# Performance work log

Measured on AMD Instinct MI355X. Metric: run time of the kernel, lower is better.

Reference implementation:

```python
import jax, jax.numpy as jnp
import numpy as np

B, H, S, D = 2, 12, 2048, 64

def setup_inputs() -> dict:
    key = jax.random.key(0)
    kq, kk, kv = jax.random.split(key, 3)
    Q = jax.random.normal(kq, (B, H, S, D), dtype=jnp.float32)
    K = jax.random.normal(kk, (B, H, S, D), dtype=jnp.float32)
    V = jax.random.normal(kv, (B, H, S, D), dtype=jnp.float32)
    return {"Q": Q, "K": K, "V": V}

def reference(Q, K, V):
    # NOTE: original code scales by sqrt(Q.shape[-2]) (the sequence length),
    # not the head dim — reproduced faithfully.
    scale = 1.0 / np.sqrt(Q.shape[-2]).astype(np.float32)
    scores = jnp.einsum('bhqd,bhkd->bhqk', Q, K) * scale  # [B,H,S,S]
    attn = jax.nn.softmax(scores, axis=-1)
    context = jnp.einsum('bhqk,bhkd->bhqd', attn, V)      # [B,H,S,D]
    # torch .squeeze(-1) only removes the last dim if it is size 1; D=64 so no-op
    return context
```

## Files before the change

kernel.cpp:

```cpp
#include <hip/hip_runtime.h>
#include <math.h>
#include <stdint.h>

#define BATCH 2
#define NH 12
#define SEQ 2048
#define HD 64
#define TQ 64
#define TK 64
#define NHEADS (BATCH*NH)
#define NIT (SEQ / TK)

typedef short bf16x8 __attribute__((ext_vector_type(8)));
typedef float f32x4 __attribute__((ext_vector_type(4)));
typedef unsigned short us8_t __attribute__((ext_vector_type(8)));

#if __has_builtin(__builtin_amdgcn_exp2f)
#define EXP2F(x) __builtin_amdgcn_exp2f(x)
#else
#define EXP2F(x) exp2f(x)
#endif

static __device__ __forceinline__ unsigned short f2bf(float f) {
    unsigned int u = __float_as_uint(f);
    u += 0x7fffu + ((u >> 16) & 1u);
    return (unsigned short)(u >> 16);
}

static __device__ __forceinline__ void async_cp16(const void* g, void* l) {
    __builtin_amdgcn_global_load_lds(
        (const __attribute__((address_space(1))) void*)g,
        (__attribute__((address_space(3))) void*)(uintptr_t)l,
        16, 0, 0);
}

__global__ __launch_bounds__(256)
void prep_kv(const float* __restrict__ K, const float* __restrict__ V,
             unsigned short* __restrict__ Kb, unsigned short* __restrict__ Vtb) {
    const int bh = blockIdx.x >> 5;
    const int s0 = (blockIdx.x & 31) * 64;
    const int tid = threadIdx.x;

    const float* Ksrc = K + ((size_t)bh * SEQ + s0) * HD;
    unsigned short* Kdst = Kb + ((size_t)bh * SEQ + s0) * HD;
    #pragma unroll
    for (int i = 0; i < 2; ++i) {
        int e0 = (tid + 256 * i) * 8;
        float4 a = *(const float4*)&Ksrc[e0];
        float4 b = *(const float4*)&Ksrc[e0 + 4];
        us8_t r = { f2bf(a.x), f2bf(a.y), f2bf(a.z), f2bf(a.w),
                    f2bf(b.x), f2bf(b.y), f2bf(b.z), f2bf(b.w) };
        *(us8_t*)&Kdst[e0] = r;
    }

    const float* Vsrc = V + ((size_t)bh * SEQ + s0) * HD;
    unsigned short* Vdst = Vtb + (size_t)bh * HD * SEQ;
    const int n  = tid & 63;
    const int cg = tid >> 6;
    #pragma unroll
    for (int i = 0; i < 4; ++i) {
        int c4 = (cg + 4 * i) * 4;
        float4 v = *(const float4*)&Vsrc[(size_t)n * HD + c4];
        Vdst[(size_t)(c4 + 0) * SEQ + s0 + n] = f2bf(v.x);
        Vdst[(size_t)(c4 + 1) * SEQ + s0 + n] = f2bf(v.y);
        Vdst[(size_t)(c4 + 2) * SEQ + s0 + n] = f2bf(v.z);
        Vdst[(size_t)(c4 + 3) * SEQ + s0 + n] = f2bf(v.w);
    }
}

__global__ __launch_bounds__(256)
void fa_main(const float* __restrict__ Q,
             const unsigned short* __restrict__ Kb,
             const unsigned short* __restrict__ Vtb,
             float* __restrict__ O, float qs) {
    const int x  = blockIdx.x & 7;
    const int t  = blockIdx.x >> 3;
    const int bh = x + 8 * (t % 3);
    const int qt = t / 3;
    const int q0 = qt * TQ;

    __shared__ unsigned short Qs[TQ * HD];
    __shared__ unsigned short Kdb[2][TK * HD];
    __shared__ unsigned short Vdb[2][HD * TK];
    __shared__ unsigned short Ps[4][16][72];

    const int tid   = threadIdx.x;
    const int w     = tid >> 6;
    const int lane  = tid & 63;
    const int col   = lane & 15;
    const int quad  = lane >> 4;
    const int rloc  = lane >> 3;
    const int cphys = lane & 7;
    const int swz   = col & 7;
    const int R     = w * 16;

    const float*          Qh = Q   + ((size_t)bh * SEQ + q0) * HD;
    const unsigned short* Kh = Kb  + (size_t)bh * SEQ * HD;
    const unsigned short* Vh = Vtb + (size_t)bh * HD * SEQ;

    #pragma unroll
    for (int i = 0; i < 2; ++i) {
        int c   = tid * 2 + i;
        int row = c >> 3;
        int ch  = c & 7;
        const float* src = &Qh[(size_t)row * HD + ch * 8];
        float4 a = *(const float4*)&src[0];
        float4 b = *(const float4*)&src[4];
        us8_t r = { f2bf(a.x*qs), f2bf(a.y*qs), f2bf(a.z*qs), f2bf(a.w*qs),
                    f2bf(b.x*qs), f2bf(b.y*qs), f2bf(b.z*qs), f2bf(b.w*qs) };
        *(us8_t*)&Qs[row * HD + ((ch ^ (row & 7)) * 8)] = r;
    }

    {
        async_cp16(Kh + (size_t)(0 + R     + rloc) * HD  + (cphys ^ rloc) * 8, &Kdb[0][ R      * HD]);
        async_cp16(Kh + (size_t)(0 + R + 8 + rloc) * HD  + (cphys ^ rloc) * 8, &Kdb[0][(R + 8) * HD]);
        async_cp16(Vh + (size_t)(R     + rloc) * SEQ + 0 + (cphys ^ rloc) * 8, &Vdb[0][ R      * TK]);
        async_cp16(Vh + (size_t)(R + 8 + rloc) * SEQ + 0 + (cphys ^ rloc) * 8, &Vdb[0][(R + 8) * TK]);
    }
    __syncthreads();

    bf16x8 aq0 = *(const bf16x8*)&Qs[(R + col) * HD + ((quad       ^ swz) * 8)];
    bf16x8 aq1 = *(const bf16x8*)&Qs[(R + col) * HD + (((quad + 4) ^ swz) * 8)];

    f32x4 o[4];
    #pragma unroll
    for (int nt = 0; nt < 4; ++nt) o[nt] = (f32x4){0.f, 0.f, 0.f, 0.f};
    float lsum[4] = {0.f, 0.f, 0.f, 0.f};

    for (int it = 0; it < NIT; ++it) {
        const int cur = it & 1;
        if (it + 1 < NIT) {
            const int nb  = cur ^ 1;
            const int kv0 = (it + 1) * TK;
            async_cp16(Kh + (size_t)(kv0 + R     + rloc) * HD  + (cphys ^ rloc) * 8, &Kdb[nb][ R      * HD]);
            async_cp16(Kh + (size_t)(kv0 + R + 8 + rloc) * HD  + (cphys ^ rloc) * 8, &Kdb[nb][(R + 8) * HD]);
            async_cp16(Vh + (size_t)(R     + rloc) * SEQ + kv0 + (cphys ^ rloc) * 8, &Vdb[nb][ R      * TK]);
            async_cp16(Vh + (size_t)(R + 8 + rloc) * SEQ + kv0 + (cphys ^ rloc) * 8, &Vdb[nb][(R + 8) * TK]);
        }
        const unsigned short* Ks = Kdb[cur];
        const unsigned short* Vs = Vdb[cur];

        f32x4 sc[4];
        #pragma unroll
        for (int nt = 0; nt < 4; ++nt) {
            const int br = nt * 16 + col;
            bf16x8 bk0 = *(const bf16x8*)&Ks[br * HD + ((quad       ^ swz) * 8)];
            bf16x8 bk1 = *(const bf16x8*)&Ks[br * HD + (((quad + 4) ^ swz) * 8)];
            f32x4 z = {0.f, 0.f, 0.f, 0.f};
            z = __builtin_amdgcn_mfma_f32_16x16x32_bf16(aq0, bk0, z, 0, 0, 0);
            z = __builtin_amdgcn_mfma_f32_16x16x32_bf16(aq1, bk1, z, 0, 0, 0);
            sc[nt] = z;
        }

        #pragma unroll
        for (int nt = 0; nt < 4; ++nt) {
            #pragma unroll
            for (int r = 0; r < 4; ++r) {
                float p = EXP2F(sc[nt][r]);
                lsum[r] += p;
                Ps[w][quad * 4 + r][nt * 16 + col] = f2bf(p);
            }
        }

        bf16x8 ap0 = *(const bf16x8*)&Ps[w][col][quad * 8];
        bf16x8 ap1 = *(const bf16x8*)&Ps[w][col][32 + quad * 8];
        #pragma unroll
        for (int nt = 0; nt < 4; ++nt) {
            const int br = nt * 16 + col;
            bf16x8 bv0 = *(const bf16x8*)&Vs[br * TK + ((quad       ^ swz) * 8)];
            bf16x8 bv1 = *(const bf16x8*)&Vs[br * TK + (((quad + 4) ^ swz) * 8)];
            o[nt] = __builtin_amdgcn_mfma_f32_16x16x32_bf16(ap0, bv0, o[nt], 0, 0, 0);
            o[nt] = __builtin_amdgcn_mfma_f32_16x16x32_bf16(ap1, bv1, o[nt], 0, 0, 0);
        }

        __syncthreads();
    }

    #pragma unroll
    for (int off = 1; off < 16; off <<= 1)
        #pragma unroll
        for (int r = 0; r < 4; ++r) lsum[r] += __shfl_xor(lsum[r], off, 64);

    float inv[4];
    #pragma unroll
    for (int r = 0; r < 4; ++r) inv[r] = 1.0f / lsum[r];

    float* Oh = O + ((size_t)bh * SEQ + q0) * HD;
    #pragma unroll
    for (int r = 0; r < 4; ++r) {
        size_t row = (size_t)(R + quad * 4 + r) * HD;
        Oh[row +  0 + col] = o[0][r] * inv[r];
        Oh[row + 16 + col] = o[1][r] * inv[r];
        Oh[row + 32 + col] = o[2][r] * inv[r];
        Oh[row + 48 + col] = o[3][r] * inv[r];
    }
}

#define PAD 8
#define LSTR (HD + PAD)

__global__ __launch_bounds__(256)
void fa_fwd_fb(const float* __restrict__ Q, const float* __restrict__ K,
               const float* __restrict__ V, float* __restrict__ O) {
    const int x  = blockIdx.x & 7;
    const int t  = blockIdx.x >> 3;
    const int bh = x + 8 * (t % 3);
    const int qt = t / 3;
    const int q0 = qt * TQ;
    const long base = (long)bh * SEQ * HD;

    __shared__ unsigned short Qs[TQ][LSTR];
    __shared__ unsigned short Ks2[TK][LSTR];
    __shared__ unsigned short Vt[HD][TK + PAD];
    __shared__ unsigned short Ps2[4][16][LSTR];

    const int tid  = threadIdx.x;
    const int wave = tid >> 6;
    const int lane = tid & 63;
    const int col  = lane & 15;
    const int quad = lane >> 4;
    const int m0   = wave * 16;

    #pragma unroll
    for (int i = 0; i < 4; ++i) {
        int idx = tid + 256 * i;
        int row = idx >> 4;
        int c4  = (idx & 15) * 4;
        float4 v = *(const float4*)&Q[base + (long)(q0 + row) * HD + c4];
        ushort4 b = { f2bf(v.x), f2bf(v.y), f2bf(v.z), f2bf(v.w) };
        *(ushort4*)&Qs[row][c4] = b;
    }
    __syncthreads();

    bf16x8 aq0 = *(const bf16x8*)&Qs[m0 + col][quad * 8];
    bf16x8 aq1 = *(const bf16x8*)&Qs[m0 + col][32 + quad * 8];

    f32x4 o0 = {0.f,0.f,0.f,0.f}, o1 = o0, o2 = o0, o3 = o0;
    float l[4] = {0.f, 0.f, 0.f, 0.f};
    const float scale = 0.022097086912079608f;

    for (int kv0 = 0; kv0 < SEQ; kv0 += TK) {
        __syncthreads();
        #pragma unroll
        for (int i = 0; i < 4; ++i) {
            int idx = tid + 256 * i;
            int row = idx >> 4;
            int c4  = (idx & 15) * 4;
            float4 kv = *(const float4*)&K[base + (long)(kv0 + row) * HD + c4];
            ushort4 kb = { f2bf(kv.x), f2bf(kv.y), f2bf(kv.z), f2bf(kv.w) };
            *(ushort4*)&Ks2[row][c4] = kb;
            float4 vv = *(const float4*)&V[base + (long)(kv0 + row) * HD + c4];
            Vt[c4 + 0][row] = f2bf(vv.x);
            Vt[c4 + 1][row] = f2bf(vv.y);
            Vt[c4 + 2][row] = f2bf(vv.z);
            Vt[c4 + 3][row] = f2bf(vv.w);
        }
        __syncthreads();

        f32x4 sc[4];
        #pragma unroll
        for (int n = 0; n < 4; ++n) {
            bf16x8 b0 = *(const bf16x8*)&Ks2[n * 16 + col][quad * 8];
            bf16x8 b1 = *(const bf16x8*)&Ks2[n * 16 + col][32 + quad * 8];
            f32x4 acc = {0.f,0.f,0.f,0.f};
            acc = __builtin_amdgcn_mfma_f32_16x16x32_bf16(aq0, b0, acc, 0, 0, 0);
            acc = __builtin_amdgcn_mfma_f32_16x16x32_bf16(aq1, b1, acc, 0, 0, 0);
            sc[n] = acc;
        }

        float tsum[4] = {0.f, 0.f, 0.f, 0.f};
        #pragma unroll
        for (int n = 0; n < 4; ++n) {
            #pragma unroll
            for (int r = 0; r < 4; ++r) {
                float p = __expf(sc[n][r] * scale);
                tsum[r] += p;
                Ps2[wave][quad * 4 + r][n * 16 + col] = f2bf(p);
            }
        }
        #pragma unroll
        for (int off = 1; off < 16; off <<= 1) {
            #pragma unroll
            for (int r = 0; r < 4; ++r) tsum[r] += __shfl_xor(tsum[r], off, 64);
        }
        #pragma unroll
        for (int r = 0; r < 4; ++r) l[r] += tsum[r];

        bf16x8 ap0 = *(const bf16x8*)&Ps2[wave][col][quad * 8];
        bf16x8 ap1 = *(const bf16x8*)&Ps2[wave][col][32 + quad * 8];
        #pragma unroll
        for (int n = 0; n < 4; ++n) {
            bf16x8 b0 = *(const bf16x8*)&Vt[n * 16 + col][quad * 8];
            bf16x8 b1 = *(const bf16x8*)&Vt[n * 16 + col][32 + quad * 8];
            f32x4* op = (n == 0) ? &o0 : (n == 1) ? &o1 : (n == 2) ? &o2 : &o3;
            *op = __builtin_amdgcn_mfma_f32_16x16x32_bf16(ap0, b0, *op, 0, 0, 0);
            *op = __builtin_amdgcn_mfma_f32_16x16x32_bf16(ap1, b1, *op, 0, 0, 0);
        }
    }

    float inv[4];
    #pragma unroll
    for (int r = 0; r < 4; ++r) inv[r] = 1.0f / l[r];
    #pragma unroll
    for (int r = 0; r < 4; ++r) {
        long row = base + (long)(q0 + m0 + quad * 4 + r) * HD;
        O[row +  0 + col] = o0[r] * inv[r];
        O[row + 16 + col] = o1[r] * inv[r];
        O[row + 32 + col] = o2[r] * inv[r];
        O[row + 48 + col] = o3[r] * inv[r];
    }
}

extern "C" void kernel_launch(void* const* d_in, const int* in_sizes, int n_in,
                              void* d_out, int out_size, void* d_ws, size_t ws_size,
                              hipStream_t stream) {
    const float* Q = (const float*)d_in[0];
    const float* K = (const float*)d_in[1];
    const float* V = (const float*)d_in[2];
    float* O = (float*)d_out;

    const size_t tensorElems = (size_t)NHEADS * SEQ * HD;
    const size_t need = 2 * tensorElems * sizeof(unsigned short);

    if (ws_size >= need) {
        unsigned short* Kb  = (unsigned short*)d_ws;
        unsigned short* Vtb = Kb + tensorElems;
        const float qs = (float)(1.4426950408889634 / sqrt(2048.0));
        prep_kv<<<dim3(NHEADS * (SEQ / 64)), dim3(256), 0, stream>>>(K, V, Kb, Vtb);
        fa_main<<<dim3(NHEADS * (SEQ / TQ)), dim3(256), 0, stream>>>(Q, Kb, Vtb, O, qs);
    } else {
        fa_fwd_fb<<<dim3(NHEADS * (SEQ / TQ)), dim3(256), 0, stream>>>(Q, K, V, O);
    }
}
```

Baseline: 130.5 us.

## Use two-wave blocks with 32 query rows per wave and single-buffered KV

Main attention kernel now runs 128 threads per block, each wave handling 32 query rows (two M tiles), so every K/V fragment loaded from LDS feeds twice as many MFMAs. The QK product is computed transposed (K as A operand), which lets P be written with packed bf16x4 stores. Q is converted to bf16 and pre-scaled in the prep kernel, and its LDS buffer is reused for P. K/V double buffering is dropped in favour of a single buffer reloaded between two barriers, which exposes load latency unless other resident blocks hide it.

```diff
diff --git a/kernel.cpp b/kernel.cpp
--- a/kernel.cpp
+++ b/kernel.cpp
@@ -1,4 +1,5 @@
 #include <hip/hip_runtime.h>
+#include <hip/hip_bf16.h>
 #include <math.h>
 #include <stdint.h>
 
@@ -27,6 +28,11 @@
     return (unsigned short)(u >> 16);
 }
 
+static __device__ __forceinline__ unsigned int pack2bf(float a, float b) {
+    __hip_bfloat162 v = __float22bfloat162_rn(float2{a, b});
+    return *(unsigned int*)&v;
+}
+
 static __device__ __forceinline__ void async_cp16(const void* g, void* l) {
     __builtin_amdgcn_global_load_lds(
         (const __attribute__((address_space(1))) void*)g,
@@ -35,25 +41,31 @@
 }
 
 __global__ __launch_bounds__(256)
-void prep_kv(const float* __restrict__ K, const float* __restrict__ V,
-             unsigned short* __restrict__ Kb, unsigned short* __restrict__ Vtb) {
+void prep_qkv(const float* __restrict__ Q, const float* __restrict__ K,
+              const float* __restrict__ V,
+              unsigned short* __restrict__ Qb, unsigned short* __restrict__ Kb,
+              unsigned short* __restrict__ Vtb, float qs) {
     const int bh = blockIdx.x >> 5;
     const int s0 = (blockIdx.x & 31) * 64;
     const int tid = threadIdx.x;
-
-    const float* Ksrc = K + ((size_t)bh * SEQ + s0) * HD;
-    unsigned short* Kdst = Kb + ((size_t)bh * SEQ + s0) * HD;
+    const size_t off = ((size_t)bh * SEQ + s0) * HD;
+
     #pragma unroll
     for (int i = 0; i < 2; ++i) {
-        int e0 = (tid + 256 * i) * 8;
-        float4 a = *(const float4*)&Ksrc[e0];
-        float4 b = *(const float4*)&Ksrc[e0 + 4];
-        us8_t r = { f2bf(a.x), f2bf(a.y), f2bf(a.z), f2bf(a.w),
-                    f2bf(b.x), f2bf(b.y), f2bf(b.z), f2bf(b.w) };
-        *(us8_t*)&Kdst[e0] = r;
-    }
-
-    const float* Vsrc = V + ((size_t)bh * SEQ + s0) * HD;
+        size_t e0 = off + (size_t)(tid + 256 * i) * 8;
+        float4 a = *(const float4*)&Q[e0];
+        float4 b = *(const float4*)&Q[e0 + 4];
+        us8_t rq = { f2bf(a.x*qs), f2bf(a.y*qs), f2bf(a.z*qs), f2bf(a.w*qs),
+                     f2bf(b.x*qs), f2bf(b.y*qs), f2bf(b.z*qs), f2bf(b.w*qs) };
+        *(us8_t*)&Qb[e0] = rq;
+        float4 c = *(const float4*)&K[e0];
+        float4 d = *(const float4*)&K[e0 + 4];
+        us8_t rk = { f2bf(c.x), f2bf(c.y), f2bf(c.z), f2bf(c.w),
+                     f2bf(d.x), f2bf(d.y), f2bf(d.z), f2bf(d.w) };
+        *(us8_t*)&Kb[e0] = rk;
+    }
+
+    const float* Vsrc = V + off;
     unsigned short* Vdst = Vtb + (size_t)bh * HD * SEQ;
     const int n  = tid & 63;
     const int cg = tid >> 6;
@@ -68,131 +80,146 @@
     }
 }
 
-__global__ __launch_bounds__(256)
-void fa_main(const float* __restrict__ Q,
+__global__ __launch_bounds__(128)
+void fa_main(const unsigned short* __restrict__ Qb,
              const unsigned short* __restrict__ Kb,
              const unsigned short* __restrict__ Vtb,
-             float* __restrict__ O, float qs) {
+             float* __restrict__ O) {
     const int x  = blockIdx.x & 7;
     const int t  = blockIdx.x >> 3;
     const int bh = x + 8 * (t % 3);
     const int qt = t / 3;
     const int q0 = qt * TQ;
 
-    __shared__ unsigned short Qs[TQ * HD];
-    __shared__ unsigned short Kdb[2][TK * HD];
-    __shared__ unsigned short Vdb[2][HD * TK];
-    __shared__ unsigned short Ps[4][16][72];
-
-    const int tid   = threadIdx.x;
-    const int w     = tid >> 6;
-    const int lane  = tid & 63;
-    const int col   = lane & 15;
-    const int quad  = lane >> 4;
-    const int rloc  = lane >> 3;
-    const int cphys = lane & 7;
-    const int swz   = col & 7;
-    const int R     = w * 16;
-
-    const float*          Qh = Q   + ((size_t)bh * SEQ + q0) * HD;
+    __shared__ unsigned short Ks[TK * HD];
+    __shared__ unsigned short Vs[HD * TK];
+    __shared__ unsigned short QP[2 * 32 * 72];
+    __shared__ float Lw[2][32];
+
+    const int tid  = threadIdx.x;
+    const int w    = tid >> 6;
+    const int lane = tid & 63;
+    const int col  = lane & 15;
+    const int quad = lane >> 4;
+    const int r8   = lane >> 3;
+    const int c8   = lane & 7;
+    const int swz  = col & 7;
+
+    const unsigned short* Qh = Qb  + ((size_t)bh * SEQ + q0) * HD;
     const unsigned short* Kh = Kb  + (size_t)bh * SEQ * HD;
     const unsigned short* Vh = Vtb + (size_t)bh * HD * SEQ;
 
     #pragma unroll
-    for (int i = 0; i < 2; ++i) {
-        int c   = tid * 2 + i;
-        int row = c >> 3;
-        int ch  = c & 7;
-        const float* src = &Qh[(size_t)row * HD + ch * 8];
-        float4 a = *(const float4*)&src[0];
-        float4 b = *(const float4*)&src[4];
-        us8_t r = { f2bf(a.x*qs), f2bf(a.y*qs), f2bf(a.z*qs), f2bf(a.w*qs),
-                    f2bf(b.x*qs), f2bf(b.y*qs), f2bf(b.z*qs), f2bf(b.w*qs) };
-        *(us8_t*)&Qs[row * HD + ((ch ^ (row & 7)) * 8)] = r;
-    }
-
-    {
-        async_cp16(Kh + (size_t)(0 + R     + rloc) * HD  + (cphys ^ rloc) * 8, &Kdb[0][ R      * HD]);
-        async_cp16(Kh + (size_t)(0 + R + 8 + rloc) * HD  + (cphys ^ rloc) * 8, &Kdb[0][(R + 8) * HD]);
-        async_cp16(Vh + (size_t)(R     + rloc) * SEQ + 0 + (cphys ^ rloc) * 8, &Vdb[0][ R      * TK]);
-        async_cp16(Vh + (size_t)(R + 8 + rloc) * SEQ + 0 + (cphys ^ rloc) * 8, &Vdb[0][(R + 8) * TK]);
+    for (int i = 0; i < 4; ++i) {
+        const int R = w * 32 + i * 8;
+        async_cp16(Qh + (size_t)(R + r8) * HD + (c8 ^ r8) * 8, &QP[R * HD]);
+    }
+    #pragma unroll
+    for (int i = 0; i < 4; ++i) {
+        const int R = w * 32 + i * 8;
+        async_cp16(Kh + (size_t)(R + r8) * HD + (c8 ^ r8) * 8, &Ks[R * HD]);
+        async_cp16(Vh + (size_t)(R + r8) * SEQ + (c8 ^ r8) * 8, &Vs[R * HD]);
     }
     __syncthreads();
 
-    bf16x8 aq0 = *(const bf16x8*)&Qs[(R + col) * HD + ((quad       ^ swz) * 8)];
-    bf16x8 aq1 = *(const bf16x8*)&Qs[(R + col) * HD + (((quad + 4) ^ swz) * 8)];
-
-    f32x4 o[4];
-    #pragma unroll
-    for (int nt = 0; nt < 4; ++nt) o[nt] = (f32x4){0.f, 0.f, 0.f, 0.f};
-    float lsum[4] = {0.f, 0.f, 0.f, 0.f};
+    bf16x8 qf[2][2];
+    #pragma unroll
+    for (int mt = 0; mt < 2; ++mt)
+        #pragma unroll
+        for (int ks = 0; ks < 2; ++ks)
+            qf[mt][ks] = *(const bf16x8*)&QP[(w*32 + mt*16 + col) * HD + (((ks*4 + quad) ^ swz) * 8)];
+    __syncthreads();
+
+    unsigned short* Psw = &QP[w * 2304];
+
+    f32x4 o[2][4];
+    #pragma unroll
+    for (int mt = 0; mt < 2; ++mt)
+        #pragma unroll
+        for (int dt = 0; dt < 4; ++dt) o[mt][dt] = (f32x4){0.f, 0.f, 0.f, 0.f};
+    float lsum[2] = {0.f, 0.f};
 
     for (int it = 0; it < NIT; ++it) {
-        const int cur = it & 1;
+        f32x4 sc[2][4];
+        #pragma unroll
+        for (int nt = 0; nt < 4; ++nt) {
+            const int kr = (nt*16 + col) * HD;
+            bf16x8 kf0 = *(const bf16x8*)&Ks[kr + (((0*4 + quad) ^ swz) * 8)];
+            bf16x8 kf1 = *(const bf16x8*)&Ks[kr + (((1*4 + quad) ^ swz) * 8)];
+            #pragma unroll
+            for (int mt = 0; mt < 2; ++mt) {
+                f32x4 z = {0.f, 0.f, 0.f, 0.f};
+                z = __builtin_amdgcn_mfma_f32_16x16x32_bf16(kf0, qf[mt][0], z, 0, 0, 0);
+                z = __builtin_amdgcn_mfma_f32_16x16x32_bf16(kf1, qf[mt][1], z, 0, 0, 0);
+                sc[mt][nt] = z;
+            }
+        }
+
+        #pragma unroll
+        for (int mt = 0; mt < 2; ++mt) {
+            #pragma unroll
+            for (int nt = 0; nt < 4; ++nt) {
+                float p0 = EXP2F(sc[mt][nt][0]);
+                float p1 = EXP2F(sc[mt][nt][1]);
+                float p2 = EXP2F(sc[mt][nt][2]);
+                float p3 = EXP2F(sc[mt][nt][3]);
+                lsum[mt] += (p0 + p1) + (p2 + p3);
+                uint2 pk = { pack2bf(p0, p1), pack2bf(p2, p3) };
+                *(uint2*)&Psw[(mt*16 + col) * 72 + nt*16 + quad*4] = pk;
+            }
+        }
+
+        bf16x8 pf[2][2];
+        #pragma unroll
+        for (int mt = 0; mt < 2; ++mt)
+            #pragma unroll
+            for (int ks = 0; ks < 2; ++ks)
+                pf[mt][ks] = *(const bf16x8*)&Psw[(mt*16 + col) * 72 + ks*32 + quad*8];
+        #pragma unroll
+        for (int dt = 0; dt < 4; ++dt) {
+            const int vr = (dt*16 + col) * HD;
+            bf16x8 vf0 = *(const bf16x8*)&Vs[vr + (((0*4 + quad) ^ swz) * 8)];
+            bf16x8 vf1 = *(const bf16x8*)&Vs[vr + (((1*4 + quad) ^ swz) * 8)];
+            #pragma unroll
+            for (int mt = 0; mt < 2; ++mt) {
+                o[mt][dt] = __builtin_amdgcn_mfma_f32_16x16x32_bf16(pf[mt][0], vf0, o[mt][dt], 0, 0, 0);
+                o[mt][dt] = __builtin_amdgcn_mfma_f32_16x16x32_bf16(pf[mt][1], vf1, o[mt][dt], 0, 0, 0);
+            }
+        }
+
+        __syncthreads();
         if (it + 1 < NIT) {
-            const int nb  = cur ^ 1;
             const int kv0 = (it + 1) * TK;
-            async_cp16(Kh + (size_t)(kv0 + R     + rloc) * HD  + (cphys ^ rloc) * 8, &Kdb[nb][ R      * HD]);
-            async_cp16(Kh + (size_t)(kv0 + R + 8 + rloc) * HD  + (cphys ^ rloc) * 8, &Kdb[nb][(R + 8) * HD]);
-            async_cp16(Vh + (size_t)(R     + rloc) * SEQ + kv0 + (cphys ^ rloc) * 8, &Vdb[nb][ R      * TK]);
-            async_cp16(Vh + (size_t)(R + 8 + rloc) * SEQ + kv0 + (cphys ^ rloc) * 8, &Vdb[nb][(R + 8) * TK]);
-        }
-        const unsigned short* Ks = Kdb[cur];
-        const unsigned short* Vs = Vdb[cur];
-
-        f32x4 sc[4];
-        #pragma unroll
-        for (int nt = 0; nt < 4; ++nt) {
-            const int br = nt * 16 + col;
-            bf16x8 bk0 = *(const bf16x8*)&Ks[br * HD + ((quad       ^ swz) * 8)];
-            bf16x8 bk1 = *(const bf16x8*)&Ks[br * HD + (((quad + 4) ^ swz) * 8)];
-            f32x4 z = {0.f, 0.f, 0.f, 0.f};
-            z = __builtin_amdgcn_mfma_f32_16x16x32_bf16(aq0, bk0, z, 0, 0, 0);
-            z = __builtin_amdgcn_mfma_f32_16x16x32_bf16(aq1, bk1, z, 0, 0, 0);
-            sc[nt] = z;
-        }
-
-        #pragma unroll
-        for (int nt = 0; nt < 4; ++nt) {
-            #pragma unroll
-            for (int r = 0; r < 4; ++r) {
-                float p = EXP2F(sc[nt][r]);
-                lsum[r] += p;
-                Ps[w][quad * 4 + r][nt * 16 + col] = f2bf(p);
-            }
-        }
-
-        bf16x8 ap0 = *(const bf16x8*)&Ps[w][col][quad * 8];
-        bf16x8 ap1 = *(const bf16x8*)&Ps[w][col][32 + quad * 8];
-        #pragma unroll
-        for (int nt = 0; nt < 4; ++nt) {
-            const int br = nt * 16 + col;
-            bf16x8 bv0 = *(const bf16x8*)&Vs[br * TK + ((quad       ^ swz) * 8)];
-            bf16x8 bv1 = *(const bf16x8*)&Vs[br * TK + (((quad + 4) ^ swz) * 8)];
-            o[nt] = __builtin_amdgcn_mfma_f32_16x16x32_bf16(ap0, bv0, o[nt], 0, 0, 0);
-            o[nt] = __builtin_amdgcn_mfma_f32_16x16x32_bf16(ap1, bv1, o[nt], 0, 0, 0);
-        }
-
+            #pragma unroll
+            for (int i = 0; i < 4; ++i) {
+                const int R = w * 32 + i * 8;
+                async_cp16(Kh + (size_t)(kv0 + R + r8) * HD  + (c8 ^ r8) * 8, &Ks[R * HD]);
+                async_cp16(Vh + (size_t)(R + r8) * SEQ + kv0 + (c8 ^ r8) * 8, &Vs[R * HD]);
+            }
+        }
         __syncthreads();
     }
 
     #pragma unroll
-    for (int off = 1; off < 16; off <<= 1)
-        #pragma unroll
-        for (int r = 0; r < 4; ++r) lsum[r] += __shfl_xor(lsum[r], off, 64);
-
-    float inv[4];
-    #pragma unroll
-    for (int r = 0; r < 4; ++r) inv[r] = 1.0f / lsum[r];
-
-    float* Oh = O + ((size_t)bh * SEQ + q0) * HD;
-    #pragma unroll
-    for (int r = 0; r < 4; ++r) {
-        size_t row = (size_t)(R + quad * 4 + r) * HD;
-        Oh[row +  0 + col] = o[0][r] * inv[r];
-        Oh[row + 16 + col] = o[1][r] * inv[r];
-        Oh[row + 32 + col] = o[2][r] * inv[r];
-        Oh[row + 48 + col] = o[3][r] * inv[r];
+    for (int mt = 0; mt < 2; ++mt) {
+        lsum[mt] += __shfl_xor(lsum[mt], 16, 64);
+        lsum[mt] += __shfl_xor(lsum[mt], 32, 64);
+    }
+    if (quad == 0) {
+        Lw[w][col]      = lsum[0];
+        Lw[w][16 + col] = lsum[1];
+    }
+    float* Oh = O + ((size_t)bh * SEQ + q0 + w*32) * HD;
+    #pragma unroll
+    for (int mt = 0; mt < 2; ++mt) {
+        #pragma unroll
+        for (int r = 0; r < 4; ++r) {
+            const int row = mt*16 + quad*4 + r;
+            float inv = 1.0f / Lw[w][row];
+            #pragma unroll
+            for (int dt = 0; dt < 4; ++dt)
+                Oh[(size_t)row * HD + dt*16 + col] = o[mt][dt][r] * inv;
+        }
     }
 }
 
@@ -320,14 +347,15 @@
     float* O = (float*)d_out;
 
     const size_t tensorElems = (size_t)NHEADS * SEQ * HD;
-    const size_t need = 2 * tensorElems * sizeof(unsigned short);
+    const size_t need = 3 * tensorElems * sizeof(unsigned short);
 
     if (ws_size >= need) {
-        unsigned short* Kb  = (unsigned short*)d_ws;
+        unsigned short* Qb  = (unsigned short*)d_ws;
+        unsigned short* Kb  = Qb + tensorElems;
         unsigned short* Vtb = Kb + tensorElems;
         const float qs = (float)(1.4426950408889634 / sqrt(2048.0));
-        prep_kv<<<dim3(NHEADS * (SEQ / 64)), dim3(256), 0, stream>>>(K, V, Kb, Vtb);
-        fa_main<<<dim3(NHEADS * (SEQ / TQ)), dim3(256), 0, stream>>>(Q, Kb, Vtb, O, qs);
+        prep_qkv<<<dim3(NHEADS * (SEQ / 64)), dim3(256), 0, stream>>>(Q, K, V, Qb, Kb, Vtb, qs);
+        fa_main<<<dim3(NHEADS * (SEQ / TQ)), dim3(128), 0, stream>>>(Qb, Kb, Vtb, O);
     } else {
         fa_fwd_fb<<<dim3(NHEADS * (SEQ / TQ)), dim3(256), 0, stream>>>(Q, K, V, O);
     }
```

Measured after the change: 140.1 us. 1.07x slower.
